# Kernel optimization log

Hardware: AMD Instinct MI355X
Metric: run time of the kernel (lower is better)

The kernel has to match this reference:

```python
import jax, jax.numpy as jnp
import numpy as np

B, T, D, H = 2048, 512, 32, 64


def _gru_layer(x, W_ih, W_hh, b_ih, b_hh):
    # x: [B, T, Din]; W_ih: [3H, Din]; W_hh: [3H, H]; gate order r, z, n (PyTorch).
    xp = jnp.einsum('btd,gd->btg', x, W_ih) + b_ih  # precompute input projections [B,T,3H]

    def step(h, xt):
        gh = h @ W_hh.T + b_hh                      # [B,3H]
        ir, iz, inn = jnp.split(xt, 3, axis=-1)
        hr, hz, hn = jnp.split(gh, 3, axis=-1)
        r = jax.nn.sigmoid(ir + hr)
        z = jax.nn.sigmoid(iz + hz)
        n = jnp.tanh(inn + r * hn)
        h_new = (1.0 - z) * n + z * h
        return h_new, h_new

    h0 = jnp.zeros((x.shape[0], W_hh.shape[1]), dtype=x.dtype)
    _, ys = jax.lax.scan(step, h0, xp.transpose(1, 0, 2))  # ys: [T,B,H]
    return ys.transpose(1, 0, 2)                           # [B,T,H]


def setup_inputs() -> dict:
    key = jax.random.key(0)
    ks = jax.random.split(key, 12)
    s_in = 1.0 / np.sqrt(H)
    u = lambda k, shp: jax.random.uniform(k, shp, jnp.float32, -s_in, s_in)
    return {
        'x': jax.random.normal(ks[0], (B, T, D), jnp.float32),
        'W_ih0': u(ks[1], (3 * H, D)),  'W_hh0': u(ks[2], (3 * H, H)),
        'b_ih0': u(ks[3], (3 * H,)),    'b_hh0': u(ks[4], (3 * H,)),
        'W_ih1': u(ks[5], (3 * H, H)),  'W_hh1': u(ks[6], (3 * H, H)),
        'b_ih1': u(ks[7], (3 * H,)),    'b_hh1': u(ks[8], (3 * H,)),
        'fc_w': u(ks[9], (1, H)),       'fc_b': u(ks[10], (1,)),
    }


def reference(x, W_ih0, W_hh0, b_ih0, b_hh0, W_ih1, W_hh1, b_ih1, b_hh1, fc_w, fc_b):
    # 2-layer GRU (eval mode: inter-layer dropout is identity) + linear head on last step.
    h1 = _gru_layer(x, W_ih0, W_hh0, b_ih0, b_hh0)   # [B,T,H]
    h2 = _gru_layer(h1, W_ih1, W_hh1, b_ih1, b_hh1)  # [B,T,H]
    out = h2[:, -1, :] @ fc_w.T + fc_b               # [B,1]
    return out[:, 0]                                  # [B]
```

## Files before the change

### kernel.cpp

```cpp
#include <hip/hip_runtime.h>

#define Bsz  2048
#define Tlen 512
#define Din  32
#define Hd   64
#define BT   16
#define HS   72
#define BUFE 2048

typedef _Float16 half8 __attribute__((ext_vector_type(8)));
typedef _Float16 half4 __attribute__((ext_vector_type(4)));
typedef float    f32x4 __attribute__((ext_vector_type(4)));

#define MFMA(a, b, c) __builtin_amdgcn_mfma_f32_16x16x32_f16((a), (b), (c), 0, 0, 0)

#define BARRIER()                                              \
  do {                                                         \
    asm volatile("s_waitcnt lgkmcnt(0)" ::: "memory");         \
    __builtin_amdgcn_s_barrier();                              \
  } while (0)

__device__ __forceinline__ half8 load8s(const float* p, float s) {
    half8 r;
#pragma unroll
    for (int j = 0; j < 8; ++j) r[j] = (_Float16)(p[j] * s);
    return r;
}
__device__ __forceinline__ half8 cvt8(float4 a, float4 b) {
    half8 r;
    r[0] = (_Float16)a.x; r[1] = (_Float16)a.y; r[2] = (_Float16)a.z; r[3] = (_Float16)a.w;
    r[4] = (_Float16)b.x; r[5] = (_Float16)b.y; r[6] = (_Float16)b.z; r[7] = (_Float16)b.w;
    return r;
}

__device__ __forceinline__ half4 gate_upd(const f32x4& gr, const f32x4& gz,
                                          const f32x4& anx, const f32x4& anh,
                                          float hst[4]) {
    half4 pk;
#pragma unroll
    for (int r = 0; r < 4; ++r) {
        float Er = __builtin_amdgcn_exp2f(gr[r]);
        float rr = __builtin_amdgcn_rcpf(1.0f + Er);
        float yy = anx[r] + rr * anh[r];
        float En = __builtin_amdgcn_exp2f(yy);
        float Ez = __builtin_amdgcn_exp2f(gz[r]);
        float num = Ez * (1.0f - En) + hst[r] * (1.0f + En);
        float den = (1.0f + Ez) * (1.0f + En);
        hst[r] = num * __builtin_amdgcn_rcpf(den);
        pk[r] = (_Float16)hst[r];
    }
    return pk;
}

__global__ __launch_bounds__(512)
void gru_fused(const float* __restrict__ x,
               const float* __restrict__ Wih0, const float* __restrict__ Whh0,
               const float* __restrict__ bih0, const float* __restrict__ bhh0,
               const float* __restrict__ Wih1, const float* __restrict__ Whh1,
               const float* __restrict__ bih1, const float* __restrict__ bhh1,
               const float* __restrict__ fcw,  const float* __restrict__ fcb,
               float* __restrict__ out)
{
    __shared__ _Float16 arena[4 * BUFE];
    __shared__ float hfin[BT][Hd];

    const int tid  = threadIdx.x;
    const int lane = tid & 63;
    const int wave = tid >> 6;
    const int grp  = wave >> 2;
    const int wg   = wave & 3;
    const int m    = lane & 15;
    const int quad = lane >> 4;
    const int col  = (wg << 4) + m;
    const int gc   = (wg << 4) + (quad << 2);
    const int b0   = blockIdx.x << 4;

    for (int idx = tid; idx < 4 * BUFE; idx += 512) arena[idx] = (_Float16)0.f;

    const float sRZ = -1.44269504f;
    const float sN  = -2.88539008f;
    const int rdoff = m * HS + quad * 8;
    const int wroff = m * HS + gc;
    float hst[4] = {0.f, 0.f, 0.f, 0.f};

    half8 wx[2][3], wh[2][3];
    f32x4 brz0v, brz1v, binv, bhnv;
    if (grp == 0) {
        wx[0][0] = load8s(Wih0 + (      col) * Din + quad * 8, sRZ);
        wx[0][1] = load8s(Wih0 + ( 64 + col) * Din + quad * 8, sRZ);
        wx[0][2] = load8s(Wih0 + (128 + col) * Din + quad * 8, sN);
#pragma unroll
        for (int kb = 0; kb < 2; ++kb) {
            wh[kb][0] = load8s(Whh0 + (      col) * Hd + kb * 32 + quad * 8, sRZ);
            wh[kb][1] = load8s(Whh0 + ( 64 + col) * Hd + kb * 32 + quad * 8, sRZ);
            wh[kb][2] = load8s(Whh0 + (128 + col) * Hd + kb * 32 + quad * 8, sN);
        }
#pragma unroll
        for (int r = 0; r < 4; ++r) {
            brz0v[r] = sRZ * (bih0[gc + r] + bhh0[gc + r]);
            brz1v[r] = sRZ * (bih0[64 + gc + r] + bhh0[64 + gc + r]);
            binv[r]  = sN * bih0[128 + gc + r];
            bhnv[r]  = sN * bhh0[128 + gc + r];
        }
    } else {
#pragma unroll
        for (int kb = 0; kb < 2; ++kb) {
            wx[kb][0] = load8s(Wih1 + (      col) * Hd + kb * 32 + quad * 8, sRZ);
            wx[kb][1] = load8s(Wih1 + ( 64 + col) * Hd + kb * 32 + quad * 8, sRZ);
            wx[kb][2] = load8s(Wih1 + (128 + col) * Hd + kb * 32 + quad * 8, sN);
            wh[kb][0] = load8s(Whh1 + (      col) * Hd + kb * 32 + quad * 8, sRZ);
            wh[kb][1] = load8s(Whh1 + ( 64 + col) * Hd + kb * 32 + quad * 8, sRZ);
            wh[kb][2] = load8s(Whh1 + (128 + col) * Hd + kb * 32 + quad * 8, sN);
        }
#pragma unroll
        for (int r = 0; r < 4; ++r) {
            brz0v[r] = sRZ * (bih1[gc + r] + bhh1[gc + r]);
            brz1v[r] = sRZ * (bih1[64 + gc + r] + bhh1[64 + gc + r]);
            binv[r]  = sN * bih1[128 + gc + r];
            bhnv[r]  = sN * bhh1[128 + gc + r];
        }
    }

    const float* xgp = x + (size_t)(b0 + m) * (Tlen * Din) + quad * 8;
    float4 x0a, x0b, x1a, x1b;
    f32x4 xar, xaz, xan;
    if (grp == 0) {
        x0a = *(const float4*)(xgp);        x0b = *(const float4*)(xgp + 4);
        x1a = *(const float4*)(xgp + Din);  x1b = *(const float4*)(xgp + Din + 4);
        half8 ax = cvt8(x0a, x0b);
        xar = brz0v; xar = MFMA(wx[0][0], ax, xar);
        xaz = brz1v; xaz = MFMA(wx[0][1], ax, xaz);
        xan = binv;  xan = MFMA(wx[0][2], ax, xan);
        {
            const float* p = xgp + 2 * Din;
            x0a = *(const float4*)p; x0b = *(const float4*)(p + 4);
        }
    }
    half8 bx0, bx1;
    f32x4 arx, azx, anx, arh, azh, anh;

    __syncthreads();

#define REGION(I, RO, WO, XA, XB, DO1)                                   \
  do {                                                                   \
                             \
    if (grp == 0) {                                                      \
      const _Float16* s1 = arena + (RO) + rdoff;                         \
      half8 bh0 = *(const half8*)s1;                                     \
      half8 bh1 = *(const half8*)(s1 + 32);                              \
      f32x4 arh0 = {0.f,0.f,0.f,0.f}, azh0 = {0.f,0.f,0.f,0.f};          \
      f32x4 anh0 = bhnv;                                                 \
      arh0 = MFMA(wh[0][0], bh0, arh0); arh0 = MFMA(wh[1][0], bh1, arh0);\
      azh0 = MFMA(wh[0][1], bh0, azh0); azh0 = MFMA(wh[1][1], bh1, azh0);\
      anh0 = MFMA(wh[0][2], bh0, anh0); anh0 = MFMA(wh[1][2], bh1, anh0);\
      f32x4 gr = xar + arh0, gz = xaz + azh0;                            \
      half4 pk = gate_upd(gr, gz, xan, anh0, hst);                       \
      *(half4*)(arena + (WO) + wroff) = pk;                              \
    } else if (DO1) {                                                    \
      const _Float16* s2 = arena + 2 * BUFE + (RO) + rdoff;              \
      half8 bh0 = *(const half8*)s2;                                     \
      half8 bh1 = *(const half8*)(s2 + 32);                              \
      arx = brz0v; azx = brz1v; anx = binv;                              \
      arh = (f32x4){0.f,0.f,0.f,0.f}; azh = (f32x4){0.f,0.f,0.f,0.f};    \
      anh = bhnv;                                                        \
      arx = MFMA(wx[0][0], bx0, arx); arx = MFMA(wx[1][0], bx1, arx);    \
      azx = MFMA(wx[0][1], bx0, azx); azx = MFMA(wx[1][1], bx1, azx);    \
      anx = MFMA(wx[0][2], bx0, anx); anx = MFMA(wx[1][2], bx1, anx);    \
      arh = MFMA(wh[0][0], bh0, arh); arh = MFMA(wh[1][0], bh1, arh);    \
      azh = MFMA(wh[0][1], bh0, azh); azh = MFMA(wh[1][1], bh1, azh);    \
      anh = MFMA(wh[0][2], bh0, anh); anh = MFMA(wh[1][2], bh1, anh);    \
    }                                                                    \
    BARRIER();                                                           \
                             \
    if (grp == 0) {                                                      \
      half8 ax = cvt8(XA, XB);                               \
      { const int nx = ((I) + 3 < Tlen) ? (I) + 3 : Tlen - 1;            \
        const float* p = xgp + (size_t)nx * Din;                         \
        XA = *(const float4*)p; XB = *(const float4*)(p + 4); }          \
      xar = brz0v; xar = MFMA(wx[0][0], ax, xar);                        \
      xaz = brz1v; xaz = MFMA(wx[0][1], ax, xaz);                        \
      xan = binv;  xan = MFMA(wx[0][2], ax, xan);                        \
    } else {                                                             \
      if (DO1) {                                                         \
        f32x4 gr = arx + arh, gz = azx + azh;                            \
        half4 pk = gate_upd(gr, gz, anx, anh, hst);                      \
        *(half4*)(arena + 2 * BUFE + (WO) + wroff) = pk;                 \
      }                                                                  \
      const _Float16* s1n = arena + (WO) + rdoff;     \
      bx0 = *(const half8*)s1n;                                          \
      bx1 = *(const half8*)(s1n + 32);                                   \
    }                                                                    \
    BARRIER();                                                           \
  } while (0)

    REGION(0, BUFE, 0, x1a, x1b, 0);
    for (int i = 1; i + 1 < Tlen; i += 2) {
        REGION(i,     0,    BUFE, x0a, x0b, 1);
        REGION(i + 1, BUFE, 0,    x1a, x1b, 1);
    }
    REGION(Tlen - 1, 0, BUFE, x0a, x0b, 1);
#undef REGION

    if (grp == 1) {
        const _Float16* s2 = arena + 2 * BUFE + BUFE + rdoff;
        half8 bh0 = *(const half8*)s2;
        half8 bh1 = *(const half8*)(s2 + 32);
        f32x4 arx2 = brz0v, azx2 = brz1v, anx2 = binv;
        f32x4 arh2 = {0.f,0.f,0.f,0.f}, azh2 = {0.f,0.f,0.f,0.f}, anh2 = bhnv;
        arx2 = MFMA(wx[0][0], bx0, arx2); arx2 = MFMA(wx[1][0], bx1, arx2);
        azx2 = MFMA(wx[0][1], bx0, azx2); azx2 = MFMA(wx[1][1], bx1, azx2);
        anx2 = MFMA(wx[0][2], bx0, anx2); anx2 = MFMA(wx[1][2], bx1, anx2);
        arh2 = MFMA(wh[0][0], bh0, arh2); arh2 = MFMA(wh[1][0], bh1, arh2);
        azh2 = MFMA(wh[0][1], bh0, azh2); azh2 = MFMA(wh[1][1], bh1, azh2);
        anh2 = MFMA(wh[0][2], bh0, anh2); anh2 = MFMA(wh[1][2], bh1, anh2);
        f32x4 gr = arx2 + arh2, gz = azx2 + azh2;
        gate_upd(gr, gz, anx2, anh2, hst);
        f32x4 fv;
#pragma unroll
        for (int r = 0; r < 4; ++r) fv[r] = hst[r];
        *(f32x4*)(&hfin[m][gc]) = fv;
    }
    __syncthreads();
    if (tid < BT) {
        float acc = fcb[0];
        for (int c = 0; c < Hd; ++c) acc += hfin[tid][c] * fcw[c];
        out[b0 + tid] = acc;
    }
}

extern "C" void kernel_launch(void* const* d_in, const int* in_sizes, int n_in,
                              void* d_out, int out_size, void* d_ws, size_t ws_size,
                              hipStream_t stream) {
    gru_fused<<<dim3(Bsz / BT), dim3(512), 0, stream>>>(
        (const float*)d_in[0],
        (const float*)d_in[1], (const float*)d_in[2],
        (const float*)d_in[3], (const float*)d_in[4],
        (const float*)d_in[5], (const float*)d_in[6],
        (const float*)d_in[7], (const float*)d_in[8],
        (const float*)d_in[9], (const float*)d_in[10],
        (float*)d_out);
}
```

Before: 487.6 us.

## Merge the two per-timestep barriers into one in the fused two-layer GRU loop

```diff
diff --git a/kernel.cpp b/kernel.cpp
--- a/kernel.cpp
+++ b/kernel.cpp
@@ -125,25 +125,19 @@
     float4 x0a, x0b, x1a, x1b;
     f32x4 xar, xaz, xan;
     if (grp == 0) {
-        x0a = *(const float4*)(xgp);        x0b = *(const float4*)(xgp + 4);
-        x1a = *(const float4*)(xgp + Din);  x1b = *(const float4*)(xgp + Din + 4);
-        half8 ax = cvt8(x0a, x0b);
+        float4 xia = *(const float4*)(xgp), xib = *(const float4*)(xgp + 4);
+        x1a = *(const float4*)(xgp + Din);      x1b = *(const float4*)(xgp + Din + 4);
+        x0a = *(const float4*)(xgp + 2 * Din);  x0b = *(const float4*)(xgp + 2 * Din + 4);
+        half8 ax = cvt8(xia, xib);
         xar = brz0v; xar = MFMA(wx[0][0], ax, xar);
         xaz = brz1v; xaz = MFMA(wx[0][1], ax, xaz);
         xan = binv;  xan = MFMA(wx[0][2], ax, xan);
-        {
-            const float* p = xgp + 2 * Din;
-            x0a = *(const float4*)p; x0b = *(const float4*)(p + 4);
-        }
-    }
-    half8 bx0, bx1;
-    f32x4 arx, azx, anx, arh, azh, anh;
+    }
 
     __syncthreads();
 
 #define REGION(I, RO, WO, XA, XB, DO1)                                   \
   do {                                                                   \
-                             \
     if (grp == 0) {                                                      \
       const _Float16* s1 = arena + (RO) + rdoff;                         \
       half8 bh0 = *(const half8*)s1;                                     \
@@ -156,23 +150,7 @@
       f32x4 gr = xar + arh0, gz = xaz + azh0;                            \
       half4 pk = gate_upd(gr, gz, xan, anh0, hst);                       \
       *(half4*)(arena + (WO) + wroff) = pk;                              \
-    } else if (DO1) {                                                    \
-      const _Float16* s2 = arena + 2 * BUFE + (RO) + rdoff;              \
-      half8 bh0 = *(const half8*)s2;                                     \
-      half8 bh1 = *(const half8*)(s2 + 32);                              \
-      arx = brz0v; azx = brz1v; anx = binv;                              \
-      arh = (f32x4){0.f,0.f,0.f,0.f}; azh = (f32x4){0.f,0.f,0.f,0.f};    \
-      anh = bhnv;                                                        \
-      arx = MFMA(wx[0][0], bx0, arx); arx = MFMA(wx[1][0], bx1, arx);    \
-      azx = MFMA(wx[0][1], bx0, azx); azx = MFMA(wx[1][1], bx1, azx);    \
-      anx = MFMA(wx[0][2], bx0, anx); anx = MFMA(wx[1][2], bx1, anx);    \
-      arh = MFMA(wh[0][0], bh0, arh); arh = MFMA(wh[1][0], bh1, arh);    \
-      azh = MFMA(wh[0][1], bh0, azh); azh = MFMA(wh[1][1], bh1, azh);    \
-      anh = MFMA(wh[0][2], bh0, anh); anh = MFMA(wh[1][2], bh1, anh);    \
-    }                                                                    \
-    BARRIER();                                                           \
-                             \
-    if (grp == 0) {                                                      \
+      \
       half8 ax = cvt8(XA, XB);                               \
       { const int nx = ((I) + 3 < Tlen) ? (I) + 3 : Tlen - 1;            \
         const float* p = xgp + (size_t)nx * Din;                         \
@@ -180,15 +158,25 @@
       xar = brz0v; xar = MFMA(wx[0][0], ax, xar);                        \
       xaz = brz1v; xaz = MFMA(wx[0][1], ax, xaz);                        \
       xan = binv;  xan = MFMA(wx[0][2], ax, xan);                        \
-    } else {                                                             \
-      if (DO1) {                                                         \
-        f32x4 gr = arx + arh, gz = azx + azh;                            \
-        half4 pk = gate_upd(gr, gz, anx, anh, hst);                      \
-        *(half4*)(arena + 2 * BUFE + (WO) + wroff) = pk;                 \
-      }                                                                  \
-      const _Float16* s1n = arena + (WO) + rdoff;     \
-      bx0 = *(const half8*)s1n;                                          \
-      bx1 = *(const half8*)(s1n + 32);                                   \
+    } else if (DO1) {                                                    \
+      const _Float16* s1 = arena + (RO) + rdoff;            \
+      const _Float16* s2 = s1 + 2 * BUFE;                   \
+      half8 bx0 = *(const half8*)s1;                                     \
+      half8 bx1 = *(const half8*)(s1 + 32);                              \
+      half8 bh0 = *(const half8*)s2;                                     \
+      half8 bh1 = *(const half8*)(s2 + 32);                              \
+      f32x4 arx = brz0v, azx = brz1v, anx = binv;                        \
+      f32x4 arh = {0.f,0.f,0.f,0.f}, azh = {0.f,0.f,0.f,0.f};            \
+      f32x4 anh = bhnv;                                                  \
+      arx = MFMA(wx[0][0], bx0, arx); arx = MFMA(wx[1][0], bx1, arx);    \
+      azx = MFMA(wx[0][1], bx0, azx); azx = MFMA(wx[1][1], bx1, azx);    \
+      anx = MFMA(wx[0][2], bx0, anx); anx = MFMA(wx[1][2], bx1, anx);    \
+      arh = MFMA(wh[0][0], bh0, arh); arh = MFMA(wh[1][0], bh1, arh);    \
+      azh = MFMA(wh[0][1], bh0, azh); azh = MFMA(wh[1][1], bh1, azh);    \
+      anh = MFMA(wh[0][2], bh0, anh); anh = MFMA(wh[1][2], bh1, anh);    \
+      f32x4 gr = arx + arh, gz = azx + azh;                              \
+      half4 pk = gate_upd(gr, gz, anx, anh, hst);                        \
+      *(half4*)(arena + 2 * BUFE + (WO) + wroff) = pk;                   \
     }                                                                    \
     BARRIER();                                                           \
   } while (0)
@@ -199,22 +187,24 @@
         REGION(i + 1, BUFE, 0,    x1a, x1b, 1);
     }
     REGION(Tlen - 1, 0, BUFE, x0a, x0b, 1);
-#undef REGION
 
     if (grp == 1) {
-        const _Float16* s2 = arena + 2 * BUFE + BUFE + rdoff;
+        const _Float16* s1 = arena + BUFE + rdoff;
+        const _Float16* s2 = s1 + 2 * BUFE;
+        half8 bx0 = *(const half8*)s1;
+        half8 bx1 = *(const half8*)(s1 + 32);
         half8 bh0 = *(const half8*)s2;
         half8 bh1 = *(const half8*)(s2 + 32);
-        f32x4 arx2 = brz0v, azx2 = brz1v, anx2 = binv;
-        f32x4 arh2 = {0.f,0.f,0.f,0.f}, azh2 = {0.f,0.f,0.f,0.f}, anh2 = bhnv;
-        arx2 = MFMA(wx[0][0], bx0, arx2); arx2 = MFMA(wx[1][0], bx1, arx2);
-        azx2 = MFMA(wx[0][1], bx0, azx2); azx2 = MFMA(wx[1][1], bx1, azx2);
-        anx2 = MFMA(wx[0][2], bx0, anx2); anx2 = MFMA(wx[1][2], bx1, anx2);
-        arh2 = MFMA(wh[0][0], bh0, arh2); arh2 = MFMA(wh[1][0], bh1, arh2);
-        azh2 = MFMA(wh[0][1], bh0, azh2); azh2 = MFMA(wh[1][1], bh1, azh2);
-        anh2 = MFMA(wh[0][2], bh0, anh2); anh2 = MFMA(wh[1][2], bh1, anh2);
-        f32x4 gr = arx2 + arh2, gz = azx2 + azh2;
-        gate_upd(gr, gz, anx2, anh2, hst);
+        f32x4 arx = brz0v, azx = brz1v, anx = binv;
+        f32x4 arh = {0.f,0.f,0.f,0.f}, azh = {0.f,0.f,0.f,0.f}, anh = bhnv;
+        arx = MFMA(wx[0][0], bx0, arx); arx = MFMA(wx[1][0], bx1, arx);
+        azx = MFMA(wx[0][1], bx0, azx); azx = MFMA(wx[1][1], bx1, azx);
+        anx = MFMA(wx[0][2], bx0, anx); anx = MFMA(wx[1][2], bx1, anx);
+        arh = MFMA(wh[0][0], bh0, arh); arh = MFMA(wh[1][0], bh1, arh);
+        azh = MFMA(wh[0][1], bh0, azh); azh = MFMA(wh[1][1], bh1, azh);
+        anh = MFMA(wh[0][2], bh0, anh); anh = MFMA(wh[1][2], bh1, anh);
+        f32x4 gr = arx + arh, gz = azx + azh;
+        gate_upd(gr, gz, anx, anh, hst);
         f32x4 fv;
 #pragma unroll
         for (int r = 0; r < 4; ++r) fv[r] = hst[r];
@@ -226,6 +216,7 @@
         for (int c = 0; c < Hd; ++c) acc += hfin[tid][c] * fcw[c];
         out[b0 + tid] = acc;
     }
+#undef REGION
 }
 
 extern "C" void kernel_launch(void* const* d_in, const int* in_sizes, int n_in,
```

Measured after the change: 464.2 us. 1.05x faster.
